# Kernel optimization log

Hardware: AMD Instinct MI355X
Metric: run time of the kernel (lower is better)

The kernel has to match this reference:

```python
import jax, jax.numpy as jnp
import numpy as np
from jax import lax

DIM = 384
NE = 8
TOPK = 2
HID = 4 * DIM
N, H, W = 32, 32, 32
EPS = 1e-6


def setup_inputs() -> dict:
    key = jax.random.key(0)
    ks = jax.random.split(key, 12)
    s = 0.02
    return {
        "input": jax.random.normal(ks[0], (N, DIM, H, W), dtype=jnp.float32),
        "dw_w": jax.random.normal(ks[1], (DIM, 1, 7, 7), dtype=jnp.float32) * s,
        "dw_b": jnp.zeros((DIM,), dtype=jnp.float32),
        "ln_g": jnp.ones((DIM,), dtype=jnp.float32),
        "ln_b": jnp.zeros((DIM,), dtype=jnp.float32),
        "gate_w": jax.random.normal(ks[2], (NE, DIM), dtype=jnp.float32) * s,
        "w1": jax.random.normal(ks[3], (NE, DIM, HID), dtype=jnp.float32) * s,
        "b1": jnp.zeros((NE, HID), dtype=jnp.float32),
        "w2": jax.random.normal(ks[4], (NE, HID, DIM), dtype=jnp.float32) * s,
        "b2": jnp.zeros((NE, DIM), dtype=jnp.float32),
        "layer_scale": jnp.ones((DIM, 1, 1), dtype=jnp.float32) * 1e-6,
    }


def reference(input, dw_w, dw_b, ln_g, ln_b, gate_w, w1, b1, w2, b2, layer_scale):
    # depthwise 7x7 conv, padding 3, groups=DIM  (NCHW)
    x = lax.conv_general_dilated(
        input, dw_w, window_strides=(1, 1), padding=((3, 3), (3, 3)),
        dimension_numbers=("NCHW", "OIHW", "NCHW"), feature_group_count=DIM,
    ) + dw_b[None, :, None, None]
    # permute to NHWC, layernorm over C with eps=1e-6
    x = jnp.transpose(x, (0, 2, 3, 1))
    mu = jnp.mean(x, axis=-1, keepdims=True)
    var = jnp.mean(jnp.square(x - mu), axis=-1, keepdims=True)
    x = (x - mu) * lax.rsqrt(var + EPS) * ln_g + ln_b

    x_flat = x.reshape(-1, DIM)  # [T, C]
    logits = x_flat @ gate_w.T   # [T, NE]
    topv, topi = lax.top_k(logits, TOPK)
    weights = jax.nn.softmax(topv, axis=-1)  # [T, K]

    # combine: out[t] = sum_e gate_e[t] * Expert_e(x_flat[t]), gate nonzero only for top-k
    out = jnp.zeros_like(x_flat)
    for e in range(NE):
        we = jnp.sum(jnp.where(topi == e, weights, 0.0), axis=-1)  # [T]
        h = jax.nn.gelu(x_flat @ w1[e] + b1[e], approximate=False)
        y = h @ w2[e] + b2[e]
        out = out + y * we[:, None]

    out = out.reshape(N, H, W, DIM)
    out = jnp.transpose(out, (0, 3, 1, 2))  # back to NCHW
    out = layer_scale[None] * out           # [C,1,1] broadcast
    # stochastic_depth prob 0.0 -> identity
    return input + out
```

## Files before the change

### kernel.cpp

```cpp
#include <hip/hip_runtime.h>
#include <hip/hip_bf16.h>
#include <hip/hip_fp8.h>

typedef __attribute__((ext_vector_type(4))) float  f32x4;
typedef __attribute__((ext_vector_type(8))) unsigned short u16x8;
typedef __attribute__((ext_vector_type(4))) unsigned short u16x4;
typedef long long f8x8;

#define DIM 384
#define NE 8
#define HID 1536
#define NB 32
#define HW 1024
#define T_TOK 32768

__device__ __forceinline__ unsigned short f2bf(float f) {
    unsigned int u = __float_as_uint(f);
    u = (u + 0x7fffu + ((u >> 16) & 1u)) >> 16;
    return (unsigned short)u;
}
__device__ __forceinline__ float bf2f(unsigned short u) {
    return __uint_as_float((unsigned int)u << 16);
}
__device__ __forceinline__ unsigned char f2fp8(float f) {
    __hip_fp8_e4m3 h(f);
    return (unsigned char)h.__x;
}

__global__ __launch_bounds__(256) void k_transpose8(const float* __restrict__ src,
                                                    unsigned char* __restrict__ dst,
                                                    int R, int C) {
    int b = blockIdx.x;
    int ctiles = C >> 5;
    int rtiles = R >> 5;
    int ct = b % ctiles;
    int rt = (b / ctiles) % rtiles;
    int e  = b / (ctiles * rtiles);
    __shared__ float t[32][33];
    int tid = threadIdx.x;
    const float* s = src + (size_t)e * R * C;
    unsigned char* d = dst + (size_t)e * C * R;
#pragma unroll
    for (int k = 0; k < 4; ++k) {
        int idx = k * 256 + tid;
        int rr = idx >> 5, cc = idx & 31;
        t[rr][cc] = s[(size_t)(rt * 32 + rr) * C + ct * 32 + cc];
    }
    __syncthreads();
    int cc = tid >> 3, r4 = tid & 7;
    unsigned int pk = 0;
#pragma unroll
    for (int i = 0; i < 4; ++i)
        pk |= (unsigned int)f2fp8(t[r4 * 4 + i][cc]) << (8 * i);
    *(unsigned int*)&d[(size_t)(ct * 32 + cc) * R + rt * 32 + r4 * 4] = pk;
}

__global__ __launch_bounds__(256) void k_conv(const float* __restrict__ in,
                                              const float* __restrict__ dw_w,
                                              const float* __restrict__ dw_b,
                                              float* __restrict__ xconv) {
    int nc = blockIdx.x;
    int c = nc % DIM;
    __shared__ float tile[38 * 38];
    __shared__ float wt[49];
    const float* plane = in + (size_t)nc * HW;
    int tid = threadIdx.x;
    if (tid < 49) wt[tid] = dw_w[c * 49 + tid];
    for (int idx = tid; idx < 38 * 38; idx += 256) {
        int ty = idx / 38, tx = idx % 38;
        int ih = ty - 3, iw = tx - 3;
        float v = 0.f;
        if ((unsigned)ih < 32u && (unsigned)iw < 32u) v = plane[ih * 32 + iw];
        tile[idx] = v;
    }
    __syncthreads();
    float bias = dw_b[c];
    int w = tid & 31, h0 = (tid >> 5) << 2;
    float acc[4] = {bias, bias, bias, bias};
#pragma unroll
    for (int iy = 0; iy < 10; ++iy) {
        float r[7];
#pragma unroll
        for (int dx = 0; dx < 7; ++dx) r[dx] = tile[(h0 + iy) * 38 + w + dx];
#pragma unroll
        for (int o = 0; o < 4; ++o) {
            int dy = iy - o;
            if (dy >= 0 && dy < 7) {
                float a = 0.f;
#pragma unroll
                for (int dx = 0; dx < 7; ++dx) a += r[dx] * wt[dy * 7 + dx];
                acc[o] += a;
            }
        }
    }
    float* outp = xconv + (size_t)nc * HW;
#pragma unroll
    for (int o = 0; o < 4; ++o) outp[(h0 + o) * 32 + w] = acc[o];
}

__global__ __launch_bounds__(256) void k_ln_gate(const float* __restrict__ xconv,
                                                 const float* __restrict__ ln_g,
                                                 const float* __restrict__ ln_b,
                                                 const float* __restrict__ gate_w,
                                                 unsigned char* __restrict__ lnout,
                                                 int* __restrict__ lists,
                                                 float* __restrict__ wgts,
                                                 int* __restrict__ counts) {
    __shared__ float xs[32][385];
    __shared__ float gw[8][384];
    __shared__ float gls[384], bls[384];
    __shared__ int hcnt[8], hbase[8];
    __shared__ int lexp[32][2];
    __shared__ int lpos[32][2];
    __shared__ float lw[32][2];

    int b = blockIdx.x;
    int n = b >> 5;
    int hw0 = (b & 31) << 5;
    int tid = threadIdx.x;

    for (int i = tid; i < 384; i += 256) { gls[i] = ln_g[i]; bls[i] = ln_b[i]; }
    for (int i = tid; i < 8 * 384; i += 256) gw[i / 384][i % 384] = gate_w[i];
    if (tid < 8) hcnt[tid] = 0;

    const float* base = xconv + (size_t)n * DIM * HW + hw0;
#pragma unroll
    for (int k = 0; k < 48; ++k) {
        int idx = k * 256 + tid;
        int c = idx >> 5, j = idx & 31;
        xs[j][c] = base[(size_t)c * HW + j];
    }
    __syncthreads();

    int tok = tid >> 3, jj = tid & 7;
    float sum = 0.f, sq = 0.f;
#pragma unroll
    for (int k = 0; k < 48; ++k) {
        float v = xs[tok][jj + 8 * k];
        sum += v; sq += v * v;
    }
#pragma unroll
    for (int m = 1; m < 8; m <<= 1) { sum += __shfl_xor(sum, m); sq += __shfl_xor(sq, m); }
    float mu = sum * (1.f / 384.f);
    float var = sq * (1.f / 384.f) - mu * mu;
    float rstd = rsqrtf(var + 1e-6f);

    int tglob = n * HW + hw0 + tok;
    float p[8] = {0, 0, 0, 0, 0, 0, 0, 0};
#pragma unroll
    for (int k = 0; k < 48; ++k) {
        int c = jj + 8 * k;
        float v = (xs[tok][c] - mu) * rstd * gls[c] + bls[c];
        lnout[(size_t)tglob * DIM + c] = f2fp8(v);
#pragma unroll
        for (int e = 0; e < 8; ++e) p[e] += v * gw[e][c];
    }
#pragma unroll
    for (int e = 0; e < 8; ++e)
#pragma unroll
        for (int m = 1; m < 8; m <<= 1) p[e] += __shfl_xor(p[e], m);

    if (jj == 0) {
        int i0 = 0; float v0 = p[0];
#pragma unroll
        for (int e = 1; e < 8; ++e) if (p[e] > v0) { v0 = p[e]; i0 = e; }
        int i1 = -1; float v1 = -1e30f;
#pragma unroll
        for (int e = 0; e < 8; ++e) if (e != i0 && p[e] > v1) { v1 = p[e]; i1 = e; }
        float w0 = 1.f / (1.f + __expf(v1 - v0));
        float w1 = 1.f - w0;
        lexp[tok][0] = i0; lexp[tok][1] = i1;
        lw[tok][0] = w0;  lw[tok][1] = w1;
        lpos[tok][0] = atomicAdd(&hcnt[i0], 1);
        lpos[tok][1] = atomicAdd(&hcnt[i1], 1);
    }
    __syncthreads();
    if (tid < 8) hbase[tid] = atomicAdd(&counts[tid], hcnt[tid]);
    __syncthreads();
    if (jj == 0) {
#pragma unroll
        for (int s = 0; s < 2; ++s) {
            int e = lexp[tok][s];
            int pos = hbase[e] + lpos[tok][s];
            lists[e * T_TOK + pos] = (tglob << 1) | s;
            wgts[e * T_TOK + pos] = lw[tok][s];
        }
    }
}

__global__ __launch_bounds__(512, 1) void k_moe(const unsigned char* __restrict__ ln,
                                                const unsigned char* __restrict__ w1t,
                                                const unsigned char* __restrict__ w2t,
                                                const float* __restrict__ b1,
                                                const float* __restrict__ b2,
                                                const int* __restrict__ lists,
                                                const float* __restrict__ wgts,
                                                const int* __restrict__ counts,
                                                unsigned short* __restrict__ y0,
                                                unsigned short* __restrict__ y1) {
    int e    = blockIdx.x & 7;
    int tile = blockIdx.x >> 3;
    int cnt = counts[e];
    if (tile * 128 >= cnt) return;

    __shared__ unsigned char X[128][400];
    __shared__ unsigned char Hs[128][136];
    __shared__ int   ents[128];
    __shared__ float wrow[128];

    int tid = threadIdx.x;
    if (tid < 128) {
        int idx = tile * 128 + tid;
        if (idx < cnt) { ents[tid] = lists[e * T_TOK + idx]; wrow[tid] = wgts[e * T_TOK + idx]; }
        else           { ents[tid] = -1;                     wrow[tid] = 0.f; }
    }
    __syncthreads();

    {
        int row = tid >> 2, q = tid & 3;
        int ent = ents[row];
        int tok = (ent < 0) ? 0 : (ent >> 1);
        const u16x8* src = (const u16x8*)(ln + (size_t)tok * DIM);
#pragma unroll
        for (int r = 0; r < 6; ++r)
            *(u16x8*)&X[row][(q + r * 4) * 16] = __builtin_nontemporal_load(&src[q + r * 4]);
    }
    __syncthreads();

    int wid = tid >> 6;
    int lane = tid & 63;
    int lr = lane & 15;
    int lq = lane >> 4;

    const unsigned char* pw1 = w1t + ((size_t)e * HID + wid * 16 + lr) * DIM + lq * 8;
    const unsigned char* pw2 = w2t + ((size_t)e * DIM + wid * 48 + lr) * HID + lq * 8;

    f32x4 Yacc[3][8] = {};

    f8x8 wall[12];
#pragma unroll
    for (int k = 0; k < 12; ++k) wall[k] = *(const f8x8*)(pw1 + k * 32);

    for (int hc = 0; hc < 12; ++hc) {
        f8x8 vall[12];
#pragma unroll
        for (int t = 0; t < 12; ++t) {
            int nj = t % 3, k2 = t / 3;
            vall[t] = *(const f8x8*)(pw2 + (size_t)nj * 16 * HID + hc * 128 + k2 * 32);
        }
        f32x4 bv = *(const f32x4*)&b1[e * HID + hc * 128 + wid * 16 + lq * 4];
        f32x4 Hf[8];
#pragma unroll
        for (int m = 0; m < 8; ++m) Hf[m] = bv;
        __builtin_amdgcn_s_setprio(1);
#pragma unroll
        for (int k = 0; k < 12; ++k) {
#pragma unroll
            for (int m = 0; m < 8; ++m) {
                f8x8 a = *(const f8x8*)&X[m * 16 + lr][k * 32 + lq * 8];
                Hf[m] = __builtin_amdgcn_mfma_f32_16x16x32_fp8_fp8(wall[k], a, Hf[m], 0, 0, 0);
            }
        }
        __builtin_amdgcn_s_setprio(0);
        if (hc < 11) {
            const unsigned char* pn = pw1 + (size_t)(hc + 1) * 128 * DIM;
#pragma unroll
            for (int k = 0; k < 12; ++k) wall[k] = *(const f8x8*)(pn + k * 32);
        }
#pragma unroll
        for (int m = 0; m < 8; ++m) {
            unsigned int pk = 0;
#pragma unroll
            for (int r = 0; r < 4; ++r) {
                float v = Hf[m][r];
                float t = v * fmaf(v * v, -0.07135481627f, -1.5957691216f);
                float g = v * __builtin_amdgcn_rcpf(1.f + __expf(t));
                pk |= (unsigned int)f2fp8(g) << (8 * r);
            }
            *(unsigned int*)&Hs[m * 16 + lr][wid * 16 + lq * 4] = pk;
        }
        asm volatile("s_waitcnt lgkmcnt(0)" ::: "memory");
        __builtin_amdgcn_s_barrier();
        __builtin_amdgcn_sched_barrier(0);
        __builtin_amdgcn_s_setprio(1);
#pragma unroll
        for (int k2 = 0; k2 < 4; ++k2) {
#pragma unroll
            for (int m = 0; m < 8; ++m) {
                f8x8 h = *(const f8x8*)&Hs[m * 16 + lr][k2 * 32 + lq * 8];
#pragma unroll
                for (int nj = 0; nj < 3; ++nj) {
                    Yacc[nj][m] = __builtin_amdgcn_mfma_f32_16x16x32_fp8_fp8(vall[k2 * 3 + nj], h, Yacc[nj][m], 0, 0, 0);
                }
            }
        }
        __builtin_amdgcn_s_setprio(0);
        asm volatile("s_waitcnt lgkmcnt(0)" ::: "memory");
        __builtin_amdgcn_s_barrier();
        __builtin_amdgcn_sched_barrier(0);
    }

    f32x4 b2v[3];
#pragma unroll
    for (int nj = 0; nj < 3; ++nj)
        b2v[nj] = *(const f32x4*)&b2[e * DIM + wid * 48 + nj * 16 + lq * 4];
#pragma unroll
    for (int m = 0; m < 8; ++m) {
        int row = m * 16 + lr;
        int ent = ents[row];
        if (ent >= 0) {
            float wv = wrow[row];
            int tok = ent >> 1;
            unsigned short* yb = (ent & 1) ? y1 : y0;
#pragma unroll
            for (int nj = 0; nj < 3; ++nj) {
                u16x4 pk;
#pragma unroll
                for (int r = 0; r < 4; ++r)
                    pk[r] = f2bf((Yacc[nj][m][r] + b2v[nj][r]) * wv);
                *(u16x4*)(yb + (size_t)tok * DIM + wid * 48 + nj * 16 + lq * 4) = pk;
            }
        }
    }
}

__global__ __launch_bounds__(256) void k_final(const float* __restrict__ input,
                                               const float* __restrict__ ls,
                                               const unsigned short* __restrict__ y0,
                                               const unsigned short* __restrict__ y1,
                                               float* __restrict__ out) {
    int b = blockIdx.x;
    int ct = b % 12;
    int hwt = (b / 12) % 32;
    int n = b / (12 * 32);
    int c0 = ct * 32, hw0 = hwt * 32;
    __shared__ float t[32][33];
    int tid = threadIdx.x;
    int t0 = n * HW + hw0;
#pragma unroll
    for (int k = 0; k < 2; ++k) {
        int idx = k * 256 + tid;
        int tl = idx >> 4, pr = idx & 15;
        size_t o = (size_t)(t0 + tl) * DIM + c0 + pr * 2;
        unsigned int a = *(const unsigned int*)(y0 + o);
        unsigned int c = *(const unsigned int*)(y1 + o);
        t[tl][pr * 2]     = bf2f((unsigned short)a) + bf2f((unsigned short)c);
        t[tl][pr * 2 + 1] = bf2f((unsigned short)(a >> 16)) + bf2f((unsigned short)(c >> 16));
    }
    __syncthreads();
#pragma unroll
    for (int k = 0; k < 4; ++k) {
        int idx = k * 256 + tid;
        int cl = idx >> 5, j = idx & 31;
        size_t o = ((size_t)n * DIM + c0 + cl) * HW + hw0 + j;
        out[o] = input[o] + ls[c0 + cl] * t[j][cl];
    }
}

extern "C" void kernel_launch(void* const* d_in, const int* in_sizes, int n_in,
                              void* d_out, int out_size, void* d_ws, size_t ws_size,
                              hipStream_t stream) {
    const float* input  = (const float*)d_in[0];
    const float* dw_w   = (const float*)d_in[1];
    const float* dw_b   = (const float*)d_in[2];
    const float* ln_g   = (const float*)d_in[3];
    const float* ln_b   = (const float*)d_in[4];
    const float* gate_w = (const float*)d_in[5];
    const float* w1     = (const float*)d_in[6];
    const float* b1     = (const float*)d_in[7];
    const float* w2     = (const float*)d_in[8];
    const float* b2     = (const float*)d_in[9];
    const float* lscale = (const float*)d_in[10];

    const size_t SZ_PLANE = (size_t)NB * DIM * HW * 4;
    const size_t SZ_YBF   = (size_t)T_TOK * DIM * 2;
    const size_t SZ_LNB   = (size_t)T_TOK * DIM;
    const size_t SZ_W1    = (size_t)NE * DIM * HID;
    char* ws = (char*)d_ws;
    float* xconv = (float*)(ws + 0);
    unsigned short* y0 = (unsigned short*)(ws + 0);
    unsigned short* y1 = (unsigned short*)(ws + SZ_YBF);
    unsigned char* lnb = (unsigned char*)(ws + SZ_PLANE);
    unsigned char* w1t = (unsigned char*)(ws + SZ_PLANE + SZ_LNB);
    unsigned char* w2t = (unsigned char*)(ws + SZ_PLANE + SZ_LNB + SZ_W1);
    int*   lists  = (int*)(ws + SZ_PLANE + SZ_LNB + 2 * SZ_W1);
    float* wgt    = (float*)(ws + SZ_PLANE + SZ_LNB + 2 * SZ_W1 + 1048576);
    int*   counts = (int*)(ws + SZ_PLANE + SZ_LNB + 2 * SZ_W1 + 2 * 1048576);
    const size_t needed = SZ_PLANE + SZ_LNB + 2 * SZ_W1 + 2 * 1048576 + 256;
    if (ws_size < needed) return;

    hipMemsetAsync(counts, 0, 32, stream);
    k_transpose8<<<8 * 12 * 48, 256, 0, stream>>>(w1, w1t, DIM, HID);
    k_transpose8<<<8 * 48 * 12, 256, 0, stream>>>(w2, w2t, HID, DIM);
    k_conv<<<NB * DIM, 256, 0, stream>>>(input, dw_w, dw_b, xconv);
    k_ln_gate<<<T_TOK / 32, 256, 0, stream>>>(xconv, ln_g, ln_b, gate_w, lnb, lists, wgt, counts);
    k_moe<<<NE * 256, 512, 0, stream>>>(lnb, w1t, w2t, b1, b2, lists, wgt, counts, y0, y1);
    k_final<<<NB * 32 * 12, 256, 0, stream>>>(input, lscale, y0, y1, (float*)d_out);
}
```

Before: 408.2 us.

## Switch MoE expert GEMMs to 32x32x16 FP8 MFMA with token-split waves

Rewrites the expert MLP inner loops to use 32x32x16 FP8 MFMA instead of 16x16x32. The 8 waves are split into 4 hidden-column groups by 2 token halves, and the weight-fragment loads and H/Y tile layouts are remapped to match. Larger MFMA tiles reduce the LDS operand reads and weight register traffic per FLOP. In exchange, register pressure goes up with 16-wide accumulators and 24-entry weight arrays, and launch_bounds no longer pins one block per CU. The W2 fragment loads move to after the first GEMM, and the X padding changes to 392 bytes.

```diff
diff --git a/kernel.cpp b/kernel.cpp
--- a/kernel.cpp
+++ b/kernel.cpp
@@ -2,9 +2,11 @@
 #include <hip/hip_bf16.h>
 #include <hip/hip_fp8.h>
 
-typedef __attribute__((ext_vector_type(4))) float  f32x4;
+typedef __attribute__((ext_vector_type(4)))  float f32x4;
+typedef __attribute__((ext_vector_type(16))) float f32x16;
 typedef __attribute__((ext_vector_type(8))) unsigned short u16x8;
 typedef __attribute__((ext_vector_type(4))) unsigned short u16x4;
+typedef __attribute__((ext_vector_type(2))) long long ll2;
 typedef long long f8x8;
 
 #define DIM 384
@@ -188,22 +190,22 @@
     }
 }
 
-__global__ __launch_bounds__(512, 1) void k_moe(const unsigned char* __restrict__ ln,
-                                                const unsigned char* __restrict__ w1t,
-                                                const unsigned char* __restrict__ w2t,
-                                                const float* __restrict__ b1,
-                                                const float* __restrict__ b2,
-                                                const int* __restrict__ lists,
-                                                const float* __restrict__ wgts,
-                                                const int* __restrict__ counts,
-                                                unsigned short* __restrict__ y0,
-                                                unsigned short* __restrict__ y1) {
+__global__ __launch_bounds__(512) void k_moe(const unsigned char* __restrict__ ln,
+                                             const unsigned char* __restrict__ w1t,
+                                             const unsigned char* __restrict__ w2t,
+                                             const float* __restrict__ b1,
+                                             const float* __restrict__ b2,
+                                             const int* __restrict__ lists,
+                                             const float* __restrict__ wgts,
+                                             const int* __restrict__ counts,
+                                             unsigned short* __restrict__ y0,
+                                             unsigned short* __restrict__ y1) {
     int e    = blockIdx.x & 7;
     int tile = blockIdx.x >> 3;
     int cnt = counts[e];
     if (tile * 128 >= cnt) return;
 
-    __shared__ unsigned char X[128][400];
+    __shared__ unsigned char X[128][392];
     __shared__ unsigned char Hs[128][136];
     __shared__ int   ents[128];
     __shared__ float wrow[128];
@@ -220,78 +222,97 @@
         int row = tid >> 2, q = tid & 3;
         int ent = ents[row];
         int tok = (ent < 0) ? 0 : (ent >> 1);
-        const u16x8* src = (const u16x8*)(ln + (size_t)tok * DIM);
-#pragma unroll
-        for (int r = 0; r < 6; ++r)
-            *(u16x8*)&X[row][(q + r * 4) * 16] = __builtin_nontemporal_load(&src[q + r * 4]);
-    }
-    __syncthreads();
-
-    int wid = tid >> 6;
-    int lane = tid & 63;
-    int lr = lane & 15;
-    int lq = lane >> 4;
-
-    const unsigned char* pw1 = w1t + ((size_t)e * HID + wid * 16 + lr) * DIM + lq * 8;
-    const unsigned char* pw2 = w2t + ((size_t)e * DIM + wid * 48 + lr) * HID + lq * 8;
-
-    f32x4 Yacc[3][8] = {};
-
-    f8x8 wall[12];
-#pragma unroll
-    for (int k = 0; k < 12; ++k) wall[k] = *(const f8x8*)(pw1 + k * 32);
+        const ll2* src = (const ll2*)(ln + (size_t)tok * DIM);
+#pragma unroll
+        for (int r = 0; r < 6; ++r) {
+            ll2 v = src[q + r * 4];
+            int off = (q + r * 4) * 16;
+            *(f8x8*)&X[row][off]     = v.x;
+            *(f8x8*)&X[row][off + 8] = v.y;
+        }
+    }
+    __syncthreads();
+
+    int w  = tid >> 6;
+    int l  = tid & 63;
+    int l5 = l & 31;
+    int hi = l >> 5;
+    int wid = w >> 1;
+    int tg  = w & 1;
+
+    const unsigned char* pw1 = w1t + ((size_t)e * HID + wid * 32 + l5) * DIM + hi * 8;
+    const unsigned char* pw2 = w2t + ((size_t)e * DIM + wid * 96 + l5) * HID + hi * 8;
+
+    f32x16 Yacc[3][2] = {};
+
+    f8x8 wf[24];
+#pragma unroll
+    for (int ks = 0; ks < 24; ++ks) wf[ks] = *(const f8x8*)(pw1 + ks * 16);
+    __builtin_amdgcn_sched_barrier(0);
 
     for (int hc = 0; hc < 12; ++hc) {
-        f8x8 vall[12];
-#pragma unroll
-        for (int t = 0; t < 12; ++t) {
-            int nj = t % 3, k2 = t / 3;
-            vall[t] = *(const f8x8*)(pw2 + (size_t)nj * 16 * HID + hc * 128 + k2 * 32);
-        }
-        f32x4 bv = *(const f32x4*)&b1[e * HID + hc * 128 + wid * 16 + lq * 4];
-        f32x4 Hf[8];
-#pragma unroll
-        for (int m = 0; m < 8; ++m) Hf[m] = bv;
+        f32x16 hinit;
+#pragma unroll
+        for (int q = 0; q < 4; ++q) {
+            f32x4 bq = *(const f32x4*)&b1[e * HID + hc * 128 + wid * 32 + q * 8 + hi * 4];
+#pragma unroll
+            for (int i = 0; i < 4; ++i) hinit[q * 4 + i] = bq[i];
+        }
+        f32x16 Hf[2]; Hf[0] = hinit; Hf[1] = hinit;
         __builtin_amdgcn_s_setprio(1);
 #pragma unroll
-        for (int k = 0; k < 12; ++k) {
-#pragma unroll
-            for (int m = 0; m < 8; ++m) {
-                f8x8 a = *(const f8x8*)&X[m * 16 + lr][k * 32 + lq * 8];
-                Hf[m] = __builtin_amdgcn_mfma_f32_16x16x32_fp8_fp8(wall[k], a, Hf[m], 0, 0, 0);
+        for (int ks = 0; ks < 24; ++ks) {
+            f8x8 x0 = *(const f8x8*)&X[tg * 64 + l5][ks * 16 + hi * 8];
+            f8x8 x1 = *(const f8x8*)&X[tg * 64 + 32 + l5][ks * 16 + hi * 8];
+            Hf[0] = __builtin_amdgcn_mfma_f32_32x32x16_fp8_fp8(wf[ks], x0, Hf[0], 0, 0, 0);
+            Hf[1] = __builtin_amdgcn_mfma_f32_32x32x16_fp8_fp8(wf[ks], x1, Hf[1], 0, 0, 0);
+        }
+        __builtin_amdgcn_s_setprio(0);
+        __builtin_amdgcn_sched_barrier(0);
+        f8x8 vf[24];
+        {
+            const unsigned char* p2 = pw2 + hc * 128;
+#pragma unroll
+            for (int nj = 0; nj < 3; ++nj)
+#pragma unroll
+                for (int ks = 0; ks < 8; ++ks)
+                    vf[nj * 8 + ks] = *(const f8x8*)(p2 + (size_t)nj * 32 * HID + ks * 16);
+        }
+        __builtin_amdgcn_sched_barrier(0);
+#pragma unroll
+        for (int t = 0; t < 2; ++t) {
+            int tok = tg * 64 + t * 32 + l5;
+#pragma unroll
+            for (int q = 0; q < 4; ++q) {
+                unsigned int pk = 0;
+#pragma unroll
+                for (int i = 0; i < 4; ++i) {
+                    float v = Hf[t][q * 4 + i];
+                    float zz = v * fmaf(v * v, -0.07135481627f, -1.5957691216f);
+                    float g = v * __builtin_amdgcn_rcpf(1.f + __expf(zz));
+                    pk |= (unsigned int)f2fp8(g) << (8 * i);
+                }
+                *(unsigned int*)&Hs[tok][wid * 32 + q * 8 + hi * 4] = pk;
             }
         }
-        __builtin_amdgcn_s_setprio(0);
         if (hc < 11) {
             const unsigned char* pn = pw1 + (size_t)(hc + 1) * 128 * DIM;
 #pragma unroll
-            for (int k = 0; k < 12; ++k) wall[k] = *(const f8x8*)(pn + k * 32);
-        }
-#pragma unroll
-        for (int m = 0; m < 8; ++m) {
-            unsigned int pk = 0;
-#pragma unroll
-            for (int r = 0; r < 4; ++r) {
-                float v = Hf[m][r];
-                float t = v * fmaf(v * v, -0.07135481627f, -1.5957691216f);
-                float g = v * __builtin_amdgcn_rcpf(1.f + __expf(t));
-                pk |= (unsigned int)f2fp8(g) << (8 * r);
-            }
-            *(unsigned int*)&Hs[m * 16 + lr][wid * 16 + lq * 4] = pk;
-        }
+            for (int ks = 0; ks < 24; ++ks) wf[ks] = *(const f8x8*)(pn + ks * 16);
+        }
+        __builtin_amdgcn_sched_barrier(0);
         asm volatile("s_waitcnt lgkmcnt(0)" ::: "memory");
         __builtin_amdgcn_s_barrier();
         __builtin_amdgcn_sched_barrier(0);
         __builtin_amdgcn_s_setprio(1);
 #pragma unroll
-        for (int k2 = 0; k2 < 4; ++k2) {
-#pragma unroll
-            for (int m = 0; m < 8; ++m) {
-                f8x8 h = *(const f8x8*)&Hs[m * 16 + lr][k2 * 32 + lq * 8];
-#pragma unroll
-                for (int nj = 0; nj < 3; ++nj) {
-                    Yacc[nj][m] = __builtin_amdgcn_mfma_f32_16x16x32_fp8_fp8(vall[k2 * 3 + nj], h, Yacc[nj][m], 0, 0, 0);
-                }
+        for (int ks = 0; ks < 8; ++ks) {
+            f8x8 h0 = *(const f8x8*)&Hs[tg * 64 + l5][ks * 16 + hi * 8];
+            f8x8 h1 = *(const f8x8*)&Hs[tg * 64 + 32 + l5][ks * 16 + hi * 8];
+#pragma unroll
+            for (int nj = 0; nj < 3; ++nj) {
+                Yacc[nj][0] = __builtin_amdgcn_mfma_f32_32x32x16_fp8_fp8(vf[nj * 8 + ks], h0, Yacc[nj][0], 0, 0, 0);
+                Yacc[nj][1] = __builtin_amdgcn_mfma_f32_32x32x16_fp8_fp8(vf[nj * 8 + ks], h1, Yacc[nj][1], 0, 0, 0);
             }
         }
         __builtin_amdgcn_s_setprio(0);
@@ -300,25 +321,25 @@
         __builtin_amdgcn_sched_barrier(0);
     }
 
-    f32x4 b2v[3];
-#pragma unroll
-    for (int nj = 0; nj < 3; ++nj)
-        b2v[nj] = *(const f32x4*)&b2[e * DIM + wid * 48 + nj * 16 + lq * 4];
-#pragma unroll
-    for (int m = 0; m < 8; ++m) {
-        int row = m * 16 + lr;
-        int ent = ents[row];
+#pragma unroll
+    for (int t = 0; t < 2; ++t) {
+        int slot = tg * 64 + t * 32 + l5;
+        int ent = ents[slot];
         if (ent >= 0) {
-            float wv = wrow[row];
+            float wv = wrow[slot];
             int tok = ent >> 1;
             unsigned short* yb = (ent & 1) ? y1 : y0;
 #pragma unroll
             for (int nj = 0; nj < 3; ++nj) {
-                u16x4 pk;
-#pragma unroll
-                for (int r = 0; r < 4; ++r)
-                    pk[r] = f2bf((Yacc[nj][m][r] + b2v[nj][r]) * wv);
-                *(u16x4*)(yb + (size_t)tok * DIM + wid * 48 + nj * 16 + lq * 4) = pk;
+#pragma unroll
+                for (int q = 0; q < 4; ++q) {
+                    f32x4 b2q = *(const f32x4*)&b2[e * DIM + wid * 96 + nj * 32 + q * 8 + hi * 4];
+                    u16x4 pk;
+#pragma unroll
+                    for (int i = 0; i < 4; ++i)
+                        pk[i] = f2bf((Yacc[nj][t][q * 4 + i] + b2q[i]) * wv);
+                    *(u16x4*)(yb + (size_t)tok * DIM + wid * 96 + nj * 32 + q * 8 + hi * 4) = pk;
+                }
             }
         }
     }
```

After: 573.1 us. 40.4% more time.

## Software-pipeline expert weight loads with inline asm and manual vmcnt waits

Applied to the files above, without the earlier changes.

Replaces compiler-scheduled global loads of the W1 and W2 fragments in the MoE kernel with inline-asm global_load_dwordx2 calls. The next chunk's W2 fragments are prefetched after the second GEMM, and explicit s_waitcnt vmcnt(12) counters wait only for the set about to be consumed, so loads overlap MFMA work. The b1 bias is staged once into shared memory instead of being read from global memory every chunk. Manual vmcnt accounting is fragile: any other outstanding global load (for example the nontemporal X loads) can shift the counters, and the inline asm adds register pressure.

```diff
diff --git a/kernel.cpp b/kernel.cpp
--- a/kernel.cpp
+++ b/kernel.cpp
@@ -205,10 +205,12 @@
 
     __shared__ unsigned char X[128][400];
     __shared__ unsigned char Hs[128][136];
+    __shared__ float b1s[HID];
     __shared__ int   ents[128];
     __shared__ float wrow[128];
 
     int tid = threadIdx.x;
+    for (int i = tid; i < HID; i += 512) b1s[i] = b1[e * HID + i];
     if (tid < 128) {
         int idx = tile * 128 + tid;
         if (idx < cnt) { ents[tid] = lists[e * T_TOK + idx]; wrow[tid] = wgts[e * T_TOK + idx]; }
@@ -236,19 +238,21 @@
     const unsigned char* pw2 = w2t + ((size_t)e * DIM + wid * 48 + lr) * HID + lq * 8;
 
     f32x4 Yacc[3][8] = {};
-
-    f8x8 wall[12];
-#pragma unroll
-    for (int k = 0; k < 12; ++k) wall[k] = *(const f8x8*)(pw1 + k * 32);
+    f8x8 wf[12], vf[12];
+
+#pragma unroll
+    for (int k = 0; k < 12; ++k)
+        asm volatile("global_load_dwordx2 %0, %1, off"
+                     : "=v"(wf[k]) : "v"(pw1 + k * 32) : "memory");
+#pragma unroll
+    for (int t = 0; t < 12; ++t)
+        asm volatile("global_load_dwordx2 %0, %1, off"
+                     : "=v"(vf[t]) : "v"(pw2 + (size_t)(t % 3) * 16 * HID + (t / 3) * 32) : "memory");
 
     for (int hc = 0; hc < 12; ++hc) {
-        f8x8 vall[12];
-#pragma unroll
-        for (int t = 0; t < 12; ++t) {
-            int nj = t % 3, k2 = t / 3;
-            vall[t] = *(const f8x8*)(pw2 + (size_t)nj * 16 * HID + hc * 128 + k2 * 32);
-        }
-        f32x4 bv = *(const f32x4*)&b1[e * HID + hc * 128 + wid * 16 + lq * 4];
+        asm volatile("s_waitcnt vmcnt(12)" ::: "memory");
+        __builtin_amdgcn_sched_barrier(0);
+        f32x4 bv = *(const f32x4*)&b1s[hc * 128 + wid * 16 + lq * 4];
         f32x4 Hf[8];
 #pragma unroll
         for (int m = 0; m < 8; ++m) Hf[m] = bv;
@@ -258,14 +262,16 @@
 #pragma unroll
             for (int m = 0; m < 8; ++m) {
                 f8x8 a = *(const f8x8*)&X[m * 16 + lr][k * 32 + lq * 8];
-                Hf[m] = __builtin_amdgcn_mfma_f32_16x16x32_fp8_fp8(wall[k], a, Hf[m], 0, 0, 0);
+                Hf[m] = __builtin_amdgcn_mfma_f32_16x16x32_fp8_fp8(wf[k], a, Hf[m], 0, 0, 0);
             }
         }
         __builtin_amdgcn_s_setprio(0);
         if (hc < 11) {
             const unsigned char* pn = pw1 + (size_t)(hc + 1) * 128 * DIM;
 #pragma unroll
-            for (int k = 0; k < 12; ++k) wall[k] = *(const f8x8*)(pn + k * 32);
+            for (int k = 0; k < 12; ++k)
+                asm volatile("global_load_dwordx2 %0, %1, off"
+                             : "=v"(wf[k]) : "v"(pn + k * 32) : "memory");
         }
 #pragma unroll
         for (int m = 0; m < 8; ++m) {
@@ -273,8 +279,8 @@
 #pragma unroll
             for (int r = 0; r < 4; ++r) {
                 float v = Hf[m][r];
-                float t = v * fmaf(v * v, -0.07135481627f, -1.5957691216f);
-                float g = v * __builtin_amdgcn_rcpf(1.f + __expf(t));
+                float zz = v * fmaf(v * v, -0.07135481627f, -1.5957691216f);
+                float g = v * __builtin_amdgcn_rcpf(1.f + __expf(zz));
                 pk |= (unsigned int)f2fp8(g) << (8 * r);
             }
             *(unsigned int*)&Hs[m * 16 + lr][wid * 16 + lq * 4] = pk;
@@ -282,6 +288,9 @@
         asm volatile("s_waitcnt lgkmcnt(0)" ::: "memory");
         __builtin_amdgcn_s_barrier();
         __builtin_amdgcn_sched_barrier(0);
+        if (hc < 11) asm volatile("s_waitcnt vmcnt(12)" ::: "memory");
+        else         asm volatile("s_waitcnt vmcnt(0)"  ::: "memory");
+        __builtin_amdgcn_sched_barrier(0);
         __builtin_amdgcn_s_setprio(1);
 #pragma unroll
         for (int k2 = 0; k2 < 4; ++k2) {
@@ -289,12 +298,18 @@
             for (int m = 0; m < 8; ++m) {
                 f8x8 h = *(const f8x8*)&Hs[m * 16 + lr][k2 * 32 + lq * 8];
 #pragma unroll
-                for (int nj = 0; nj < 3; ++nj) {
-                    Yacc[nj][m] = __builtin_amdgcn_mfma_f32_16x16x32_fp8_fp8(vall[k2 * 3 + nj], h, Yacc[nj][m], 0, 0, 0);
-                }
+                for (int nj = 0; nj < 3; ++nj)
+                    Yacc[nj][m] = __builtin_amdgcn_mfma_f32_16x16x32_fp8_fp8(vf[k2 * 3 + nj], h, Yacc[nj][m], 0, 0, 0);
             }
         }
         __builtin_amdgcn_s_setprio(0);
+        if (hc < 11) {
+            const unsigned char* p2 = pw2 + (hc + 1) * 128;
+#pragma unroll
+            for (int t = 0; t < 12; ++t)
+                asm volatile("global_load_dwordx2 %0, %1, off"
+                             : "=v"(vf[t]) : "v"(p2 + (size_t)(t % 3) * 16 * HID + (t / 3) * 32) : "memory");
+        }
         asm volatile("s_waitcnt lgkmcnt(0)" ::: "memory");
         __builtin_amdgcn_s_barrier();
         __builtin_amdgcn_sched_barrier(0);
```

After: 413.1 us. About the same (+1.2%).

## Shrink MoE tiles to 64 tokens with 256-thread blocks and double-buffered H

Applied to the files above, without the earlier changes.

Restructures the expert FFN kernel from 128-token tiles with 8 waves to 64-token tiles with 4 waves. Each wave now covers 32 hidden and 96 output columns, and blocks are bounded for 3 per CU. Weight fragments are loaded directly inside the MFMA loops instead of being prefetched into registers. The hidden-activation buffer in shared memory is double-buffered, which removes the second barrier per chunk. The aim is more resident blocks and less per-chunk sync; the cost is halved weight reuse per tile and possibly exposed global load latency.

```diff
diff --git a/kernel.cpp b/kernel.cpp
--- a/kernel.cpp
+++ b/kernel.cpp
@@ -188,7 +188,7 @@
     }
 }
 
-__global__ __launch_bounds__(512, 1) void k_moe(const unsigned char* __restrict__ ln,
+__global__ __launch_bounds__(256, 3) void k_moe(const unsigned char* __restrict__ ln,
                                                 const unsigned char* __restrict__ w1t,
                                                 const unsigned char* __restrict__ w2t,
                                                 const float* __restrict__ b1,
@@ -201,16 +201,16 @@
     int e    = blockIdx.x & 7;
     int tile = blockIdx.x >> 3;
     int cnt = counts[e];
-    if (tile * 128 >= cnt) return;
-
-    __shared__ unsigned char X[128][400];
-    __shared__ unsigned char Hs[128][136];
-    __shared__ int   ents[128];
-    __shared__ float wrow[128];
+    if (tile * 64 >= cnt) return;
+
+    __shared__ unsigned char X[64][400];
+    __shared__ unsigned char Hs[2][64][136];
+    __shared__ int   ents[64];
+    __shared__ float wrow[64];
 
     int tid = threadIdx.x;
-    if (tid < 128) {
-        int idx = tile * 128 + tid;
+    if (tid < 64) {
+        int idx = tile * 64 + tid;
         if (idx < cnt) { ents[tid] = lists[e * T_TOK + idx]; wrow[tid] = wgts[e * T_TOK + idx]; }
         else           { ents[tid] = -1;                     wrow[tid] = 0.f; }
     }
@@ -232,80 +232,82 @@
     int lr = lane & 15;
     int lq = lane >> 4;
 
-    const unsigned char* pw1 = w1t + ((size_t)e * HID + wid * 16 + lr) * DIM + lq * 8;
-    const unsigned char* pw2 = w2t + ((size_t)e * DIM + wid * 48 + lr) * HID + lq * 8;
-
-    f32x4 Yacc[3][8] = {};
-
-    f8x8 wall[12];
-#pragma unroll
-    for (int k = 0; k < 12; ++k) wall[k] = *(const f8x8*)(pw1 + k * 32);
+    const unsigned char* pw1 = w1t + ((size_t)e * HID + wid * 32 + lr) * DIM + lq * 8;
+    const unsigned char* pw2 = w2t + ((size_t)e * DIM + wid * 96 + lr) * HID + lq * 8;
+
+    f32x4 Yacc[6][4] = {};
 
     for (int hc = 0; hc < 12; ++hc) {
-        f8x8 vall[12];
-#pragma unroll
-        for (int t = 0; t < 12; ++t) {
-            int nj = t % 3, k2 = t / 3;
-            vall[t] = *(const f8x8*)(pw2 + (size_t)nj * 16 * HID + hc * 128 + k2 * 32);
-        }
-        f32x4 bv = *(const f32x4*)&b1[e * HID + hc * 128 + wid * 16 + lq * 4];
-        f32x4 Hf[8];
-#pragma unroll
-        for (int m = 0; m < 8; ++m) Hf[m] = bv;
+        int buf = hc & 1;
+        const unsigned char* q1 = pw1 + (size_t)hc * 128 * DIM;
+        f32x4 bv0 = *(const f32x4*)&b1[e * HID + hc * 128 + wid * 32 + lq * 4];
+        f32x4 bv1 = *(const f32x4*)&b1[e * HID + hc * 128 + wid * 32 + 16 + lq * 4];
+        f32x4 Hf[4][2];
+#pragma unroll
+        for (int m = 0; m < 4; ++m) { Hf[m][0] = bv0; Hf[m][1] = bv1; }
         __builtin_amdgcn_s_setprio(1);
 #pragma unroll
         for (int k = 0; k < 12; ++k) {
-#pragma unroll
-            for (int m = 0; m < 8; ++m) {
-                f8x8 a = *(const f8x8*)&X[m * 16 + lr][k * 32 + lq * 8];
-                Hf[m] = __builtin_amdgcn_mfma_f32_16x16x32_fp8_fp8(wall[k], a, Hf[m], 0, 0, 0);
+            f8x8 w0 = *(const f8x8*)(q1 + k * 32);
+            f8x8 w1f = *(const f8x8*)(q1 + 16 * DIM + k * 32);
+            f8x8 a0 = *(const f8x8*)&X[ 0 + lr][k * 32 + lq * 8];
+            f8x8 a1 = *(const f8x8*)&X[16 + lr][k * 32 + lq * 8];
+            f8x8 a2 = *(const f8x8*)&X[32 + lr][k * 32 + lq * 8];
+            f8x8 a3 = *(const f8x8*)&X[48 + lr][k * 32 + lq * 8];
+            Hf[0][0] = __builtin_amdgcn_mfma_f32_16x16x32_fp8_fp8(w0, a0, Hf[0][0], 0, 0, 0);
+            Hf[1][0] = __builtin_amdgcn_mfma_f32_16x16x32_fp8_fp8(w0, a1, Hf[1][0], 0, 0, 0);
+            Hf[2][0] = __builtin_amdgcn_mfma_f32_16x16x32_fp8_fp8(w0, a2, Hf[2][0], 0, 0, 0);
+            Hf[3][0] = __builtin_amdgcn_mfma_f32_16x16x32_fp8_fp8(w0, a3, Hf[3][0], 0, 0, 0);
+            Hf[0][1] = __builtin_amdgcn_mfma_f32_16x16x32_fp8_fp8(w1f, a0, Hf[0][1], 0, 0, 0);
+            Hf[1][1] = __builtin_amdgcn_mfma_f32_16x16x32_fp8_fp8(w1f, a1, Hf[1][1], 0, 0, 0);
+            Hf[2][1] = __builtin_amdgcn_mfma_f32_16x16x32_fp8_fp8(w1f, a2, Hf[2][1], 0, 0, 0);
+            Hf[3][1] = __builtin_amdgcn_mfma_f32_16x16x32_fp8_fp8(w1f, a3, Hf[3][1], 0, 0, 0);
+        }
+        __builtin_amdgcn_s_setprio(0);
+#pragma unroll
+        for (int nj = 0; nj < 2; ++nj) {
+#pragma unroll
+            for (int m = 0; m < 4; ++m) {
+                unsigned int pk = 0;
+#pragma unroll
+                for (int r = 0; r < 4; ++r) {
+                    float v = Hf[m][nj][r];
+                    float zz = v * fmaf(v * v, -0.07135481627f, -1.5957691216f);
+                    float g = v * __builtin_amdgcn_rcpf(1.f + __expf(zz));
+                    pk |= (unsigned int)f2fp8(g) << (8 * r);
+                }
+                *(unsigned int*)&Hs[buf][m * 16 + lr][wid * 32 + nj * 16 + lq * 4] = pk;
             }
-        }
-        __builtin_amdgcn_s_setprio(0);
-        if (hc < 11) {
-            const unsigned char* pn = pw1 + (size_t)(hc + 1) * 128 * DIM;
-#pragma unroll
-            for (int k = 0; k < 12; ++k) wall[k] = *(const f8x8*)(pn + k * 32);
-        }
-#pragma unroll
-        for (int m = 0; m < 8; ++m) {
-            unsigned int pk = 0;
-#pragma unroll
-            for (int r = 0; r < 4; ++r) {
-                float v = Hf[m][r];
-                float t = v * fmaf(v * v, -0.07135481627f, -1.5957691216f);
-                float g = v * __builtin_amdgcn_rcpf(1.f + __expf(t));
-                pk |= (unsigned int)f2fp8(g) << (8 * r);
-            }
-            *(unsigned int*)&Hs[m * 16 + lr][wid * 16 + lq * 4] = pk;
         }
         asm volatile("s_waitcnt lgkmcnt(0)" ::: "memory");
         __builtin_amdgcn_s_barrier();
         __builtin_amdgcn_sched_barrier(0);
+        const unsigned char* q2 = pw2 + hc * 128;
         __builtin_amdgcn_s_setprio(1);
 #pragma unroll
         for (int k2 = 0; k2 < 4; ++k2) {
-#pragma unroll
-            for (int m = 0; m < 8; ++m) {
-                f8x8 h = *(const f8x8*)&Hs[m * 16 + lr][k2 * 32 + lq * 8];
-#pragma unroll
-                for (int nj = 0; nj < 3; ++nj) {
-                    Yacc[nj][m] = __builtin_amdgcn_mfma_f32_16x16x32_fp8_fp8(vall[k2 * 3 + nj], h, Yacc[nj][m], 0, 0, 0);
-                }
+            f8x8 h0 = *(const f8x8*)&Hs[buf][ 0 + lr][k2 * 32 + lq * 8];
+            f8x8 h1 = *(const f8x8*)&Hs[buf][16 + lr][k2 * 32 + lq * 8];
+            f8x8 h2 = *(const f8x8*)&Hs[buf][32 + lr][k2 * 32 + lq * 8];
+            f8x8 h3 = *(const f8x8*)&Hs[buf][48 + lr][k2 * 32 + lq * 8];
+#pragma unroll
+            for (int nj = 0; nj < 6; ++nj) {
+                f8x8 wf = *(const f8x8*)(q2 + (size_t)nj * 16 * HID + k2 * 32);
+                Yacc[nj][0] = __builtin_amdgcn_mfma_f32_16x16x32_fp8_fp8(wf, h0, Yacc[nj][0], 0, 0, 0);
+                Yacc[nj][1] = __builtin_amdgcn_mfma_f32_16x16x32_fp8_fp8(wf, h1, Yacc[nj][1], 0, 0, 0);
+                Yacc[nj][2] = __builtin_amdgcn_mfma_f32_16x16x32_fp8_fp8(wf, h2, Yacc[nj][2], 0, 0, 0);
+                Yacc[nj][3] = __builtin_amdgcn_mfma_f32_16x16x32_fp8_fp8(wf, h3, Yacc[nj][3], 0, 0, 0);
             }
         }
         __builtin_amdgcn_s_setprio(0);
-        asm volatile("s_waitcnt lgkmcnt(0)" ::: "memory");
-        __builtin_amdgcn_s_barrier();
-        __builtin_amdgcn_sched_barrier(0);
-    }
-
-    f32x4 b2v[3];
-#pragma unroll
-    for (int nj = 0; nj < 3; ++nj)
-        b2v[nj] = *(const f32x4*)&b2[e * DIM + wid * 48 + nj * 16 + lq * 4];
-#pragma unroll
-    for (int m = 0; m < 8; ++m) {
+    }
+
+    f32x4 b2v[6];
+#pragma unroll
+    for (int nj = 0; nj < 6; ++nj)
+        b2v[nj] = *(const f32x4*)&b2[e * DIM + wid * 96 + nj * 16 + lq * 4];
+#pragma unroll
+    for (int m = 0; m < 4; ++m) {
         int row = m * 16 + lr;
         int ent = ents[row];
         if (ent >= 0) {
@@ -313,12 +315,12 @@
             int tok = ent >> 1;
             unsigned short* yb = (ent & 1) ? y1 : y0;
 #pragma unroll
-            for (int nj = 0; nj < 3; ++nj) {
+            for (int nj = 0; nj < 6; ++nj) {
                 u16x4 pk;
 #pragma unroll
                 for (int r = 0; r < 4; ++r)
                     pk[r] = f2bf((Yacc[nj][m][r] + b2v[nj][r]) * wv);
-                *(u16x4*)(yb + (size_t)tok * DIM + wid * 48 + nj * 16 + lq * 4) = pk;
+                *(u16x4*)(yb + (size_t)tok * DIM + wid * 96 + nj * 16 + lq * 4) = pk;
             }
         }
     }
@@ -394,6 +396,6 @@
     k_transpose8<<<8 * 48 * 12, 256, 0, stream>>>(w2, w2t, HID, DIM);
     k_conv<<<NB * DIM, 256, 0, stream>>>(input, dw_w, dw_b, xconv);
     k_ln_gate<<<T_TOK / 32, 256, 0, stream>>>(xconv, ln_g, ln_b, gate_w, lnb, lists, wgt, counts);
-    k_moe<<<NE * 256, 512, 0, stream>>>(lnb, w1t, w2t, b1, b2, lists, wgt, counts, y0, y1);
+    k_moe<<<NE * 512, 256, 0, stream>>>(lnb, w1t, w2t, b1, b2, lists, wgt, counts, y0, y1);
     k_final<<<NB * 32 * 12, 256, 0, stream>>>(input, lscale, y0, y1, (float*)d_out);
 }
```

Result: slower. 485.2 us (+18.9%).
